# Optimization experiments

Measured on AMD Instinct MI355X. Metric: run time of the kernel, lower is better.

## Reference

```python
import jax, jax.numpy as jnp
import numpy as np

H = 4      # num_heads
D = 256    # hidden_dim
HD = 64    # head_dim
SCALE = HD ** -0.5


def setup_inputs() -> dict:
    key = jax.random.key(0)
    ks = jax.random.split(key, 5)
    x = jax.random.normal(ks[0], (4, 4096, D), dtype=jnp.float32)
    # Linear weights stored torch-style as [out, in]; y = x @ W.T
    init = 1.0 / np.sqrt(D)
    Wq = jax.random.uniform(ks[1], (D, D), jnp.float32, -init, init)
    Wk = jax.random.uniform(ks[2], (D, D), jnp.float32, -init, init)
    Wv = jax.random.uniform(ks[3], (D, D), jnp.float32, -init, init)
    Wo = jax.random.uniform(ks[4], (D, D), jnp.float32, -init, init)
    return {"x": x, "Wq": Wq, "Wk": Wk, "Wv": Wv, "Wo": Wo}


def reference(x, Wq, Wk, Wv, Wo):
    B, S, _ = x.shape
    # projections (torch Linear: x @ W.T)
    q = (x @ Wq.T).reshape(B, S, H, HD).transpose(0, 2, 1, 3)  # [B,H,S,HD]
    k = (x @ Wk.T).reshape(B, S, H, HD).transpose(0, 2, 1, 3)
    v = (x @ Wv.T).reshape(B, S, H, HD).transpose(0, 2, 1, 3)
    scores = jnp.einsum('bhqd,bhkd->bhqk', q, k) * SCALE  # [B,H,S,S]
    causal = jnp.triu(jnp.ones((S, S), dtype=bool), k=1)
    scores = jnp.where(causal[None, None], -jnp.inf, scores)
    attn = jax.nn.softmax(scores, axis=-1)
    out = jnp.einsum('bhqk,bhkd->bhqd', attn, v)  # [B,H,S,HD]
    out = out.transpose(0, 2, 1, 3).reshape(B, S, D)
    return out @ Wo.T
```

## Files before the change

kernel.cpp:

```cpp
#include <hip/hip_runtime.h>
#include <hip/hip_bf16.h>
#include <cstdint>

using short8  = __attribute__((ext_vector_type(8))) short;
using u16x8   = __attribute__((ext_vector_type(8))) unsigned short;
using u16x4   = __attribute__((ext_vector_type(4))) unsigned short;
using f32x4   = __attribute__((ext_vector_type(4))) float;
using f32x16  = __attribute__((ext_vector_type(16))) float;

constexpr int BN = 4, HN = 4, SN = 4096, DN = 256, HD = 64;
constexpr int MROWS = BN * SN;
constexpr float QSCL = 0.18033688011112042f;

__device__ __forceinline__ unsigned short f2bf(float x) {
  union { float f; unsigned int u; } c; c.f = x;
  unsigned int u = c.u;
  return (unsigned short)((u + 0x7fffu + ((u >> 16) & 1u)) >> 16);
}
__device__ __forceinline__ float bf2f(unsigned short h) {
  union { unsigned int u; float f; } c; c.u = ((unsigned int)h) << 16;
  return c.f;
}
__device__ __forceinline__ unsigned int cvt_pk_bf16(float a, float b) {
  unsigned int r;
  asm("v_cvt_pk_bf16_f32 %0, %1, %2" : "=v"(r) : "v"(a), "v"(b));
  return r;
}
__device__ __forceinline__ void pl32swap(unsigned int& a, unsigned int& b) {
  asm volatile("v_permlane32_swap_b32 %0, %1" : "+v"(a), "+v"(b));
}

#define GLDS16(g, l)                                                  \
  __builtin_amdgcn_global_load_lds(                                   \
      (const __attribute__((address_space(1))) void*)(g),             \
      (__attribute__((address_space(3))) void*)(l), 16, 0, 0)

__global__ __launch_bounds__(256) void convert_kernel(
    const float* __restrict__ x,  const float* __restrict__ Wq,
    const float* __restrict__ Wk, const float* __restrict__ Wv,
    const float* __restrict__ Wo,
    unsigned short* __restrict__ xb, unsigned short* __restrict__ Wcat,
    unsigned short* __restrict__ Wob) {
  const long NX4 = (long)MROWS * DN / 4;
  const long NW4 = 65536 / 4;
  const long total = NX4 + 4 * NW4;
  for (long i = (long)blockIdx.x * 256 + threadIdx.x; i < total;
       i += (long)gridDim.x * 256) {
    const float* src; unsigned short* dst;
    if (i < NX4) { src = x + i * 4; dst = xb + i * 4; }
    else {
      long j = i - NX4; int w = (int)(j >> 14); long o = (j & 16383) * 4;
      src = (w == 0 ? Wq : w == 1 ? Wk : w == 2 ? Wv : Wo) + o;
      dst = (w < 3 ? Wcat + (long)w * 65536 : Wob) + o;
    }
    float4 v = *(const float4*)src;
    u16x4 pk; pk[0] = f2bf(v.x); pk[1] = f2bf(v.y);
    pk[2] = f2bf(v.z); pk[3] = f2bf(v.w);
    *(u16x4*)dst = pk;
  }
}

template <int MODE, int NBN>
__global__ __launch_bounds__(256) void gemm_kernel(
    const unsigned short* __restrict__ Abf,
    const unsigned short* __restrict__ Bbf,
    unsigned short* __restrict__ qo, unsigned short* __restrict__ ko,
    unsigned short* __restrict__ vo, float* __restrict__ out) {
  constexpr int SMEM = (MODE == 1) ? 128 * 132 * 4 : 128 * 136 * 2;
  __shared__ __align__(16) char smem[SMEM];
  unsigned short* stg = (unsigned short*)smem;

  const int tid = threadIdx.x, lane = tid & 63, wid = tid >> 6;
  const int lo = lane & 15, hi = lane >> 4;
  const int bn = blockIdx.x % NBN, bm = blockIdx.x / NBN;
  const int wm = (wid >> 1) * 64, wn = (wid & 1) * 64;
  const long arow0 = (long)bm * 128, brow0 = (long)bn * 128;

  auto stage = [&](int buf, int kt) {
    const int row = (wid * 2) * 16 + (lane >> 2);
    const int col = (lane & 3) * 8;
    const unsigned short* ga = Abf + (arow0 + row) * DN + kt * 32 + col;
    const unsigned short* gb = Bbf + (brow0 + row) * DN + kt * 32 + col;
    unsigned short* la = stg + buf * 8192 + wid * 1024;
    unsigned short* lb = la + 4096;
    GLDS16(ga, la);
    GLDS16(ga + 16 * DN, la + 512);
    GLDS16(gb, lb);
    GLDS16(gb + 16 * DN, lb + 512);
  };

  f32x4 acc[4][4];
#pragma unroll
  for (int a = 0; a < 4; ++a)
#pragma unroll
    for (int b = 0; b < 4; ++b)
#pragma unroll
      for (int e = 0; e < 4; ++e) acc[a][b][e] = 0.f;

  stage(0, 0);
#pragma unroll
  for (int kt = 0; kt < 8; ++kt) {
    const int buf = kt & 1;
    __syncthreads();
    if (kt < 7) stage(buf ^ 1, kt + 1);
    const unsigned short* sa = stg + buf * 8192;
    const unsigned short* sb = sa + 4096;
    short8 af[4], bf[4];
#pragma unroll
    for (int f = 0; f < 4; ++f) {
      af[f] = *(const short8*)(sa + (wm + f * 16 + lo) * 32 + hi * 8);
      bf[f] = *(const short8*)(sb + (wn + f * 16 + lo) * 32 + hi * 8);
    }
#pragma unroll
    for (int fn = 0; fn < 4; ++fn)
#pragma unroll
      for (int fm = 0; fm < 4; ++fm)
        acc[fn][fm] = __builtin_amdgcn_mfma_f32_16x16x32_bf16(
            bf[fn], af[fm], acc[fn][fm], 0, 0, 0);
  }
  __syncthreads();

  if constexpr (MODE == 0) {
    unsigned short* cs = (unsigned short*)smem;
    if (bn < 4) {
      const float cscl = (bn < 2) ? QSCL : 1.0f;
#pragma unroll
      for (int fn = 0; fn < 4; ++fn)
#pragma unroll
        for (int fm = 0; fm < 4; ++fm) {
          u16x4 pk;
#pragma unroll
          for (int r = 0; r < 4; ++r) pk[r] = f2bf(acc[fn][fm][r] * cscl);
          const int m = wm + fm * 16 + lo, n0 = wn + fn * 16 + hi * 4;
          *(u16x4*)(cs + m * 136 + n0) = pk;
        }
      __syncthreads();
      unsigned short* dstmat = (bn < 2) ? qo : ko;
      const int colbase = (bn & 1) * 128;
#pragma unroll
      for (int p = 0; p < 8; ++p) {
        const int ml = p * 16 + (tid >> 4), n0 = (tid & 15) * 8;
        u16x8 v = *(u16x8*)(cs + ml * 136 + n0);
        const int c = colbase + n0, h = c >> 6, hd = c & 63;
        const long m = arow0 + ml;
        const int b = (int)(m >> 12), s = (int)(m & 4095);
        *(u16x8*)(dstmat + ((long)(b * HN + h) * SN + s) * HD + hd) = v;
      }
    } else {
#pragma unroll
      for (int fn = 0; fn < 4; ++fn)
#pragma unroll
        for (int fm = 0; fm < 4; ++fm) {
          const int m = wm + fm * 16 + lo, n0 = wn + fn * 16 + hi * 4;
#pragma unroll
          for (int r = 0; r < 4; ++r)
            cs[(n0 + r) * 136 + m] = f2bf(acc[fn][fm][r]);
        }
      __syncthreads();
      const int b = (int)(arow0 >> 12), sbase = (int)(arow0 & 4095);
#pragma unroll
      for (int p = 0; p < 8; ++p) {
        const int cl = p * 16 + (tid >> 4);
        const int s0 = (tid & 15) * 8;
        u16x8 v = *(u16x8*)(cs + cl * 136 + s0);
        const int c = (bn & 1) * 128 + cl, h = c >> 6, hd = c & 63;
        *(u16x8*)(vo + ((long)((b * HN + h) * HD + hd)) * SN + sbase + s0) = v;
      }
    }
  } else {
    float* csf = (float*)smem;
#pragma unroll
    for (int fn = 0; fn < 4; ++fn)
#pragma unroll
      for (int fm = 0; fm < 4; ++fm) {
        const int m = wm + fm * 16 + lo, n0 = wn + fn * 16 + hi * 4;
        *(f32x4*)(csf + m * 132 + n0) = acc[fn][fm];
      }
    __syncthreads();
#pragma unroll
    for (int p = 0; p < 8; ++p) {
      const int ml = p * 16 + (tid >> 4), n0 = (tid & 15) * 8;
      f32x4 v0 = *(f32x4*)(csf + ml * 132 + n0);
      f32x4 v1 = *(f32x4*)(csf + ml * 132 + n0 + 4);
      float* dst = out + (arow0 + ml) * DN + bn * 128 + n0;
      *(f32x4*)dst = v0;
      *(f32x4*)(dst + 4) = v1;
    }
  }
}

template <int NSPLIT>
__global__ __launch_bounds__(256, 2) void attn_kernel(
    const unsigned short* __restrict__ Qw, const unsigned short* __restrict__ Kw,
    const unsigned short* __restrict__ VTp, unsigned short* __restrict__ Ow,
    unsigned short* __restrict__ Op, float* __restrict__ Mp,
    float* __restrict__ Lp) {
  __shared__ __align__(16) unsigned short sK[2][4096];
  __shared__ __align__(16) unsigned short sV[2][4096];

  const int tid = threadIdx.x;
  const int w = tid >> 6, lane = tid & 63;
  const int l31 = lane & 31, h5 = lane >> 5;
  const int bid = blockIdx.x;
  const int bh = (bid & 7) * 2 + ((bid >> 3) & 1);
  int c, g;
  if constexpr (NSPLIT == 2) { c = (bid >> 4) & 1; g = bid >> 5; }
  else { c = 0; g = bid >> 4; }
  const int t = 31 - g;
  const int q0 = t * 128;
  const int qw = q0 + w * 32;
  const long base = (long)bh * SN * HD;
  const int tlast = 2 * t + 1;
  const int wlast = 2 * t + (w >> 1);

  const int sr = w * 16 + (lane >> 3);
  const int gcol8 = (((lane & 7) ^ (lane >> 3)) << 3);
  auto stage = [&](int buf, int k0) {
    const unsigned short* gk = Kw + base + (long)(k0 + sr) * HD + gcol8;
    GLDS16(gk, &sK[buf][w * 1024]);
    GLDS16(gk + 8 * HD, &sK[buf][w * 1024 + 512]);
    const unsigned short* gv = VTp + base + (long)sr * SN + k0 + gcol8;
    GLDS16(gv, &sV[buf][w * 1024]);
    GLDS16(gv + 8 * SN, &sV[buf][w * 1024 + 512]);
  };

  short8 qf[4];
#pragma unroll
  for (int ks = 0; ks < 4; ++ks)
    qf[ks] = *(const short8*)(Qw + base + (long)(qw + l31) * HD + ks * 16 + h5 * 8);

  f32x16 oacc[2];
#pragma unroll
  for (int oh = 0; oh < 2; ++oh)
#pragma unroll
    for (int r = 0; r < 16; ++r) oacc[oh][r] = 0.f;
  float m_ = -INFINITY, l_ = 0.f;

  const int swz = (l31 & 7) << 3;

  stage(0, c * 64);
  __syncthreads();
  int buf = 0;
  for (int kt = c; kt <= tlast; kt += NSPLIT) {
    if (kt + NSPLIT <= tlast) stage(buf ^ 1, (kt + NSPLIT) * 64);

    if (kt <= wlast) {
      const int k0 = kt * 64;
      short8 kb[8];
#pragma unroll
      for (int s = 0; s < 2; ++s)
#pragma unroll
        for (int ks = 0; ks < 4; ++ks)
          kb[s * 4 + ks] = *(const short8*)&sK[buf][(32 * s + l31) * 64 +
                                                   (((2 * ks + h5) << 3) ^ swz)];
      f32x16 c0, c1;
#pragma unroll
      for (int r = 0; r < 16; ++r) { c0[r] = 0.f; c1[r] = 0.f; }
#pragma unroll
      for (int ks = 0; ks < 4; ++ks)
        c0 = __builtin_amdgcn_mfma_f32_32x32x16_bf16(kb[ks], qf[ks], c0, 0, 0, 0);
#pragma unroll
      for (int ks = 0; ks < 4; ++ks)
        c1 = __builtin_amdgcn_mfma_f32_32x32x16_bf16(kb[4 + ks], qf[ks], c1, 0, 0, 0);

      short8 vt0[4], vt1[4];
#pragma unroll
      for (int ks = 0; ks < 4; ++ks) {
        const int col = ((2 * ks + h5) << 3) ^ swz;
        vt0[ks] = *(const short8*)&sV[buf][l31 * 64 + col];
        vt1[ks] = *(const short8*)&sV[buf][(32 + l31) * 64 + col];
      }

      if (kt == wlast) {
        const int mb0 = k0 + 4 * h5 - qw - l31;
#pragma unroll
        for (int r = 0; r < 16; ++r) {
          const int d = (r & 3) + 8 * (r >> 2);
          if (mb0 + d > 0)      c0[r] = -INFINITY;
          if (mb0 + 32 + d > 0) c1[r] = -INFINITY;
        }
      }

      float mv[16];
#pragma unroll
      for (int r = 0; r < 16; ++r) mv[r] = fmaxf(c0[r], c1[r]);
#pragma unroll
      for (int st = 8; st >= 1; st >>= 1)
#pragma unroll
        for (int i = 0; i < st; ++i) mv[i] = fmaxf(mv[i], mv[i + st]);
      const float mx = fmaxf(mv[0], __shfl_xor(mv[0], 32, 64));

      if (__any(mx > m_ + 11.5f)) {
        const float mn = fmaxf(m_, mx);
        const float alpha = __builtin_amdgcn_exp2f(m_ - mn);
        m_ = mn;
        l_ *= alpha;
#pragma unroll
        for (int oh = 0; oh < 2; ++oh)
#pragma unroll
          for (int r = 0; r < 16; ++r) oacc[oh][r] *= alpha;
      }

#pragma unroll
      for (int r = 0; r < 16; ++r) {
        c0[r] = __builtin_amdgcn_exp2f(c0[r] - m_);
        c1[r] = __builtin_amdgcn_exp2f(c1[r] - m_);
      }
      float sv[16];
#pragma unroll
      for (int r = 0; r < 16; ++r) sv[r] = c0[r] + c1[r];
#pragma unroll
      for (int st = 8; st >= 1; st >>= 1)
#pragma unroll
        for (int i = 0; i < st; ++i) sv[i] += sv[i + st];
      l_ += sv[0] + __shfl_xor(sv[0], 32, 64);

      short8 pb[4];
#pragma unroll
      for (int s = 0; s < 2; ++s)
#pragma unroll
        for (int u = 0; u < 2; ++u) {
          unsigned int a0, a1, b0, b1;
          if (s == 0) {
            a0 = cvt_pk_bf16(c0[8 * u + 0], c0[8 * u + 1]);
            a1 = cvt_pk_bf16(c0[8 * u + 2], c0[8 * u + 3]);
            b0 = cvt_pk_bf16(c0[8 * u + 4], c0[8 * u + 5]);
            b1 = cvt_pk_bf16(c0[8 * u + 6], c0[8 * u + 7]);
          } else {
            a0 = cvt_pk_bf16(c1[8 * u + 0], c1[8 * u + 1]);
            a1 = cvt_pk_bf16(c1[8 * u + 2], c1[8 * u + 3]);
            b0 = cvt_pk_bf16(c1[8 * u + 4], c1[8 * u + 5]);
            b1 = cvt_pk_bf16(c1[8 * u + 6], c1[8 * u + 7]);
          }
          pl32swap(a0, b0);
          pl32swap(a1, b1);
          union { unsigned int u4[4]; short8 v; } pu;
          pu.u4[0] = a0; pu.u4[1] = a1; pu.u4[2] = b0; pu.u4[3] = b1;
          pb[s * 2 + u] = pu.v;
        }

#pragma unroll
      for (int ks = 0; ks < 4; ++ks) {
        oacc[0] = __builtin_amdgcn_mfma_f32_32x32x16_bf16(vt0[ks], pb[ks], oacc[0], 0, 0, 0);
        oacc[1] = __builtin_amdgcn_mfma_f32_32x32x16_bf16(vt1[ks], pb[ks], oacc[1], 0, 0, 0);
      }
    }

    __syncthreads();
    buf ^= 1;
  }

  if constexpr (NSPLIT == 1) {
    unsigned short* ob = (unsigned short*)sK;
    const float rl = 1.f / l_;
#pragma unroll
    for (int oh = 0; oh < 2; ++oh)
#pragma unroll
      for (int rq = 0; rq < 4; ++rq) {
        const int hdb = 32 * oh + 8 * rq + 4 * h5;
        const unsigned int u0 = cvt_pk_bf16(oacc[oh][4 * rq + 0] * rl,
                                            oacc[oh][4 * rq + 1] * rl);
        const unsigned int u1 = cvt_pk_bf16(oacc[oh][4 * rq + 2] * rl,
                                            oacc[oh][4 * rq + 3] * rl);
        *(uint2*)&ob[w * 2048 + l31 * 64 + (hdb ^ ((l31 & 7) << 3))] =
            make_uint2(u0, u1);
      }
    __syncthreads();
    const int b = bh >> 2, h = bh & 3;
#pragma unroll
    for (int pass = 0; pass < 4; ++pass) {
      const int idx = pass * 256 + tid;
      const int row = idx >> 3, j = idx & 7;
      const int wreg = row >> 5, qi = row & 31;
      u16x8 vv = *(u16x8*)&ob[wreg * 2048 + qi * 64 +
                              ((j * 8) ^ ((qi & 7) << 3))];
      *(u16x8*)(Ow + ((long)(b * SN + q0 + row)) * DN + h * HD + j * 8) = vv;
    }
  } else {
    const long pb0 = (long)(c * 16 + bh) * 64;
#pragma unroll
    for (int oh = 0; oh < 2; ++oh)
#pragma unroll
      for (int rq = 0; rq < 4; ++rq)
#pragma unroll
        for (int e = 0; e < 4; ++e) {
          const int hd = 32 * oh + 8 * rq + 4 * h5 + e;
          Op[(pb0 + hd) * SN + qw + l31] = f2bf(oacc[oh][4 * rq + e]);
        }
    if (h5 == 0) {
      Mp[(long)(c * 16 + bh) * SN + qw + l31] = m_;
      Lp[(long)(c * 16 + bh) * SN + qw + l31] = l_;
    }
  }
}

template <int NS>
__global__ __launch_bounds__(256) void merge_kernel(
    const unsigned short* __restrict__ Op, const float* __restrict__ Mp,
    const float* __restrict__ Lp, unsigned short* __restrict__ Ow) {
  __shared__ float wsm[NS][64];
  __shared__ __align__(16) unsigned short obuf[64][72];
  const int tid = threadIdx.x;
  const int bh = blockIdx.x >> 6;
  const int qb = (blockIdx.x & 63) * 64;
  if (tid < 64) {
    const int q = qb + tid;
    float m[NS], l[NS];
    float ms = -INFINITY;
#pragma unroll
    for (int i = 0; i < NS; ++i) {
      m[i] = Mp[(long)(i * 16 + bh) * SN + q];
      l[i] = Lp[(long)(i * 16 + bh) * SN + q];
      ms = fmaxf(ms, m[i]);
    }
    float denom = 0.f, a[NS];
#pragma unroll
    for (int i = 0; i < NS; ++i) {
      a[i] = __builtin_amdgcn_exp2f(m[i] - ms);
      denom += l[i] * a[i];
    }
    const float rl = 1.f / denom;
#pragma unroll
    for (int i = 0; i < NS; ++i) wsm[i][tid] = a[i] * rl;
  }
  __syncthreads();
#pragma unroll
  for (int pass = 0; pass < 16; ++pass) {
    const int idx = pass * 256 + tid;
    const int hd = idx >> 6, q = idx & 63;
    float acc = 0.f;
#pragma unroll
    for (int i = 0; i < NS; ++i)
      acc += bf2f(Op[((long)(i * 16 + bh) * 64 + hd) * SN + qb + q]) * wsm[i][q];
    obuf[q][hd ^ ((q & 7) << 3)] = f2bf(acc);
  }
  __syncthreads();
  const int b = bh >> 2, h = bh & 3;
#pragma unroll
  for (int pass = 0; pass < 4; ++pass) {
    const int idx = pass * 256 + tid;
    const int q = idx >> 4, hg = (idx & 15) * 4;
    uint2 v = *(uint2*)&obuf[q][hg ^ ((q & 7) << 3)];
    *(uint2*)(Ow + ((long)(b * SN + qb + q)) * DN + h * HD + hg) = v;
  }
}

extern "C" void kernel_launch(void* const* d_in, const int* in_sizes, int n_in,
                              void* d_out, int out_size, void* d_ws, size_t ws_size,
                              hipStream_t stream) {
  const float* x  = (const float*)d_in[0];
  const float* Wq = (const float*)d_in[1];
  const float* Wk = (const float*)d_in[2];
  const float* Wv = (const float*)d_in[3];
  const float* Wo = (const float*)d_in[4];
  float* out = (float*)d_out;

  const size_t per = (size_t)MROWS * DN;
  unsigned short* xb   = (unsigned short*)d_ws;
  unsigned short* Wcat = xb + per;
  unsigned short* Wob  = Wcat + 768 * 256;
  unsigned short* Qw   = Wob + 65536;
  unsigned short* Kw   = Qw + per;
  unsigned short* VTw  = Kw + per;
  unsigned short* Ow   = xb;
  const size_t base_bytes = (4 * per + 768 * 256 + 65536) * sizeof(unsigned short);
  unsigned short* Op = (unsigned short*)((char*)d_ws + base_bytes);
  float* Mp = (float*)(Op + (size_t)2 * 16 * 64 * SN);
  float* Lp = Mp + (size_t)2 * 16 * SN;
  const size_t need = base_bytes +
      (size_t)2 * 16 * 64 * SN * sizeof(unsigned short) +
      2 * (size_t)2 * 16 * SN * sizeof(float);

  convert_kernel<<<2048, 256, 0, stream>>>(x, Wq, Wk, Wv, Wo, xb, Wcat, Wob);
  gemm_kernel<0, 6><<<6 * (MROWS / 128), 256, 0, stream>>>(
      xb, Wcat, Qw, Kw, VTw, nullptr);
  if (ws_size >= need) {
    attn_kernel<2><<<1024, 256, 0, stream>>>(Qw, Kw, VTw, nullptr, Op, Mp, Lp);
    merge_kernel<2><<<16 * (SN / 64), 256, 0, stream>>>(Op, Mp, Lp, Ow);
  } else {
    attn_kernel<1><<<512, 256, 0, stream>>>(
        Qw, Kw, VTw, Ow, nullptr, nullptr, nullptr);
  }
  gemm_kernel<1, 2><<<2 * (MROWS / 128), 256, 0, stream>>>(
      Ow, Wob, nullptr, nullptr, nullptr, out);
}
```

Before: 91.73 us.

## Give each attention wave two 32-row query tiles, halving block size

The attention kernel now runs 2 waves per block instead of 4, with each wave handling 64 query rows as two 32-row sub-tiles. The K and V fragments read from LDS are shared by both sub-tiles, which halves LDS fragment reads per unit of MFMA work. The staging loop is rewritten so 128 threads still load the full 64-row K/V tiles. The cost is roughly doubled accumulator and register pressure per wave, and fewer waves per CU to hide latency, which may reduce occupancy and increase causal-imbalance idling inside a block.

```diff
diff --git a/kernel.cpp b/kernel.cpp
--- a/kernel.cpp
+++ b/kernel.cpp
@@ -190,7 +190,7 @@
 }
 
 template <int NSPLIT>
-__global__ __launch_bounds__(256, 2) void attn_kernel(
+__global__ __launch_bounds__(128, 2) void attn_kernel(
     const unsigned short* __restrict__ Qw, const unsigned short* __restrict__ Kw,
     const unsigned short* __restrict__ VTp, unsigned short* __restrict__ Ow,
     unsigned short* __restrict__ Op, float* __restrict__ Mp,
@@ -208,35 +208,115 @@
   else { c = 0; g = bid >> 4; }
   const int t = 31 - g;
   const int q0 = t * 128;
-  const int qw = q0 + w * 32;
+  const int qA = q0 + w * 64, qB = qA + 32;
   const long base = (long)bh * SN * HD;
   const int tlast = 2 * t + 1;
-  const int wlast = 2 * t + (w >> 1);
-
-  const int sr = w * 16 + (lane >> 3);
-  const int gcol8 = (((lane & 7) ^ (lane >> 3)) << 3);
+  const int wlast = 2 * t + w;
+
+  const int r8 = lane >> 3;
+  const int gcol8 = (((lane & 7) ^ r8) << 3);
   auto stage = [&](int buf, int k0) {
-    const unsigned short* gk = Kw + base + (long)(k0 + sr) * HD + gcol8;
-    GLDS16(gk, &sK[buf][w * 1024]);
-    GLDS16(gk + 8 * HD, &sK[buf][w * 1024 + 512]);
-    const unsigned short* gv = VTp + base + (long)sr * SN + k0 + gcol8;
-    GLDS16(gv, &sV[buf][w * 1024]);
-    GLDS16(gv + 8 * SN, &sV[buf][w * 1024 + 512]);
+#pragma unroll
+    for (int i = 0; i < 4; ++i) {
+      const int row = w * 32 + i * 8;
+      GLDS16(Kw + base + (long)(k0 + row + r8) * HD + gcol8,
+             &sK[buf][row * 64]);
+      GLDS16(VTp + base + (long)(row + r8) * SN + k0 + gcol8,
+             &sV[buf][row * 64]);
+    }
   };
 
-  short8 qf[4];
-#pragma unroll
-  for (int ks = 0; ks < 4; ++ks)
-    qf[ks] = *(const short8*)(Qw + base + (long)(qw + l31) * HD + ks * 16 + h5 * 8);
-
-  f32x16 oacc[2];
-#pragma unroll
-  for (int oh = 0; oh < 2; ++oh)
-#pragma unroll
-    for (int r = 0; r < 16; ++r) oacc[oh][r] = 0.f;
-  float m_ = -INFINITY, l_ = 0.f;
+  short8 qfA[4], qfB[4];
+#pragma unroll
+  for (int ks = 0; ks < 4; ++ks) {
+    qfA[ks] = *(const short8*)(Qw + base + (long)(qA + l31) * HD + ks * 16 + h5 * 8);
+    qfB[ks] = *(const short8*)(Qw + base + (long)(qB + l31) * HD + ks * 16 + h5 * 8);
+  }
+
+  f32x16 oaccA[2], oaccB[2], zro;
+#pragma unroll
+  for (int r = 0; r < 16; ++r) zro[r] = 0.f;
+  oaccA[0] = zro; oaccA[1] = zro; oaccB[0] = zro; oaccB[1] = zro;
+  float mA = -INFINITY, lA = 0.f, mB = -INFINITY, lB = 0.f;
 
   const int swz = (l31 & 7) << 3;
+
+  auto softmax_pv = [&](f32x16& c0, f32x16& c1, float& m_, float& l_,
+                        f32x16* oacc, const short8* vt0, const short8* vt1,
+                        int kt, int k0, int qw) {
+    if (kt == wlast) {
+      const int mb0 = k0 + 4 * h5 - qw - l31;
+#pragma unroll
+      for (int r = 0; r < 16; ++r) {
+        const int d = (r & 3) + 8 * (r >> 2);
+        if (mb0 + d > 0)      c0[r] = -INFINITY;
+        if (mb0 + 32 + d > 0) c1[r] = -INFINITY;
+      }
+    }
+    float mv[16];
+#pragma unroll
+    for (int r = 0; r < 16; ++r) mv[r] = fmaxf(c0[r], c1[r]);
+#pragma unroll
+    for (int st = 8; st >= 1; st >>= 1)
+#pragma unroll
+      for (int i = 0; i < st; ++i) mv[i] = fmaxf(mv[i], mv[i + st]);
+    const float mx = fmaxf(mv[0], __shfl_xor(mv[0], 32, 64));
+
+    if (__any(mx > m_ + 11.5f)) {
+      const float mn = fmaxf(m_, mx);
+      const float alpha = __builtin_amdgcn_exp2f(m_ - mn);
+      m_ = mn;
+      l_ *= alpha;
+#pragma unroll
+      for (int oh = 0; oh < 2; ++oh)
+#pragma unroll
+        for (int r = 0; r < 16; ++r) oacc[oh][r] *= alpha;
+    }
+
+#pragma unroll
+    for (int r = 0; r < 16; ++r) {
+      c0[r] = __builtin_amdgcn_exp2f(c0[r] - m_);
+      c1[r] = __builtin_amdgcn_exp2f(c1[r] - m_);
+    }
+    float sv[16];
+#pragma unroll
+    for (int r = 0; r < 16; ++r) sv[r] = c0[r] + c1[r];
+#pragma unroll
+    for (int st = 8; st >= 1; st >>= 1)
+#pragma unroll
+      for (int i = 0; i < st; ++i) sv[i] += sv[i + st];
+    l_ += sv[0] + __shfl_xor(sv[0], 32, 64);
+
+    short8 pb[4];
+#pragma unroll
+    for (int s = 0; s < 2; ++s)
+#pragma unroll
+      for (int u = 0; u < 2; ++u) {
+        unsigned int a0, a1, b0, b1;
+        if (s == 0) {
+          a0 = cvt_pk_bf16(c0[8 * u + 0], c0[8 * u + 1]);
+          a1 = cvt_pk_bf16(c0[8 * u + 2], c0[8 * u + 3]);
+          b0 = cvt_pk_bf16(c0[8 * u + 4], c0[8 * u + 5]);
+          b1 = cvt_pk_bf16(c0[8 * u + 6], c0[8 * u + 7]);
+        } else {
+          a0 = cvt_pk_bf16(c1[8 * u + 0], c1[8 * u + 1]);
+          a1 = cvt_pk_bf16(c1[8 * u + 2], c1[8 * u + 3]);
+          b0 = cvt_pk_bf16(c1[8 * u + 4], c1[8 * u + 5]);
+          b1 = cvt_pk_bf16(c1[8 * u + 6], c1[8 * u + 7]);
+        }
+        pl32swap(a0, b0);
+        pl32swap(a1, b1);
+        union { unsigned int u4[4]; short8 v; } pu;
+        pu.u4[0] = a0; pu.u4[1] = a1; pu.u4[2] = b0; pu.u4[3] = b1;
+        pb[s * 2 + u] = pu.v;
+      }
+
+#pragma unroll
+    for (int ks = 0; ks < 4; ++ks) {
+      oacc[0] = __builtin_amdgcn_mfma_f32_32x32x16_bf16(vt0[ks], pb[ks], oacc[0], 0, 0, 0);
+      oacc[1] = __builtin_amdgcn_mfma_f32_32x32x16_bf16(vt1[ks], pb[ks], oacc[1], 0, 0, 0);
+    }
+  };
 
   stage(0, c * 64);
   __syncthreads();
@@ -253,15 +333,18 @@
         for (int ks = 0; ks < 4; ++ks)
           kb[s * 4 + ks] = *(const short8*)&sK[buf][(32 * s + l31) * 64 +
                                                    (((2 * ks + h5) << 3) ^ swz)];
-      f32x16 c0, c1;
-#pragma unroll
-      for (int r = 0; r < 16; ++r) { c0[r] = 0.f; c1[r] = 0.f; }
-#pragma unroll
-      for (int ks = 0; ks < 4; ++ks)
-        c0 = __builtin_amdgcn_mfma_f32_32x32x16_bf16(kb[ks], qf[ks], c0, 0, 0, 0);
-#pragma unroll
-      for (int ks = 0; ks < 4; ++ks)
-        c1 = __builtin_amdgcn_mfma_f32_32x32x16_bf16(kb[4 + ks], qf[ks], c1, 0, 0, 0);
+      f32x16 cA0, cA1, cB0, cB1;
+      cA0 = __builtin_amdgcn_mfma_f32_32x32x16_bf16(kb[0], qfA[0], zro, 0, 0, 0);
+      cA1 = __builtin_amdgcn_mfma_f32_32x32x16_bf16(kb[4], qfA[0], zro, 0, 0, 0);
+      cB0 = __builtin_amdgcn_mfma_f32_32x32x16_bf16(kb[0], qfB[0], zro, 0, 0, 0);
+      cB1 = __builtin_amdgcn_mfma_f32_32x32x16_bf16(kb[4], qfB[0], zro, 0, 0, 0);
+#pragma unroll
+      for (int ks = 1; ks < 4; ++ks) {
+        cA0 = __builtin_amdgcn_mfma_f32_32x32x16_bf16(kb[ks], qfA[ks], cA0, 0, 0, 0);
+        cA1 = __builtin_amdgcn_mfma_f32_32x32x16_bf16(kb[4 + ks], qfA[ks], cA1, 0, 0, 0);
+        cB0 = __builtin_amdgcn_mfma_f32_32x32x16_bf16(kb[ks], qfB[ks], cB0, 0, 0, 0);
+        cB1 = __builtin_amdgcn_mfma_f32_32x32x16_bf16(kb[4 + ks], qfB[ks], cB1, 0, 0, 0);
+      }
 
       short8 vt0[4], vt1[4];
 #pragma unroll
@@ -271,79 +354,8 @@
         vt1[ks] = *(const short8*)&sV[buf][(32 + l31) * 64 + col];
       }
 
-      if (kt == wlast) {
-        const int mb0 = k0 + 4 * h5 - qw - l31;
-#pragma unroll
-        for (int r = 0; r < 16; ++r) {
-          const int d = (r & 3) + 8 * (r >> 2);
-          if (mb0 + d > 0)      c0[r] = -INFINITY;
-          if (mb0 + 32 + d > 0) c1[r] = -INFINITY;
-        }
-      }
-
-      float mv[16];
-#pragma unroll
-      for (int r = 0; r < 16; ++r) mv[r] = fmaxf(c0[r], c1[r]);
-#pragma unroll
-      for (int st = 8; st >= 1; st >>= 1)
-#pragma unroll
-        for (int i = 0; i < st; ++i) mv[i] = fmaxf(mv[i], mv[i + st]);
-      const float mx = fmaxf(mv[0], __shfl_xor(mv[0], 32, 64));
-
-      if (__any(mx > m_ + 11.5f)) {
-        const float mn = fmaxf(m_, mx);
-        const float alpha = __builtin_amdgcn_exp2f(m_ - mn);
-        m_ = mn;
-        l_ *= alpha;
-#pragma unroll
-        for (int oh = 0; oh < 2; ++oh)
-#pragma unroll
-          for (int r = 0; r < 16; ++r) oacc[oh][r] *= alpha;
-      }
-
-#pragma unroll
-      for (int r = 0; r < 16; ++r) {
-        c0[r] = __builtin_amdgcn_exp2f(c0[r] - m_);
-        c1[r] = __builtin_amdgcn_exp2f(c1[r] - m_);
-      }
-      float sv[16];
-#pragma unroll
-      for (int r = 0; r < 16; ++r) sv[r] = c0[r] + c1[r];
-#pragma unroll
-      for (int st = 8; st >= 1; st >>= 1)
-#pragma unroll
-        for (int i = 0; i < st; ++i) sv[i] += sv[i + st];
-      l_ += sv[0] + __shfl_xor(sv[0], 32, 64);
-
-      short8 pb[4];
-#pragma unroll
-      for (int s = 0; s < 2; ++s)
-#pragma unroll
-        for (int u = 0; u < 2; ++u) {
-          unsigned int a0, a1, b0, b1;
-          if (s == 0) {
-            a0 = cvt_pk_bf16(c0[8 * u + 0], c0[8 * u + 1]);
-            a1 = cvt_pk_bf16(c0[8 * u + 2], c0[8 * u + 3]);
-            b0 = cvt_pk_bf16(c0[8 * u + 4], c0[8 * u + 5]);
-            b1 = cvt_pk_bf16(c0[8 * u + 6], c0[8 * u + 7]);
-          } else {
-            a0 = cvt_pk_bf16(c1[8 * u + 0], c1[8 * u + 1]);
-            a1 = cvt_pk_bf16(c1[8 * u + 2], c1[8 * u + 3]);
-            b0 = cvt_pk_bf16(c1[8 * u + 4], c1[8 * u + 5]);
-            b1 = cvt_pk_bf16(c1[8 * u + 6], c1[8 * u + 7]);
-          }
-          pl32swap(a0, b0);
-          pl32swap(a1, b1);
-          union { unsigned int u4[4]; short8 v; } pu;
-          pu.u4[0] = a0; pu.u4[1] = a1; pu.u4[2] = b0; pu.u4[3] = b1;
-          pb[s * 2 + u] = pu.v;
-        }
-
-#pragma unroll
-      for (int ks = 0; ks < 4; ++ks) {
-        oacc[0] = __builtin_amdgcn_mfma_f32_32x32x16_bf16(vt0[ks], pb[ks], oacc[0], 0, 0, 0);
-        oacc[1] = __builtin_amdgcn_mfma_f32_32x32x16_bf16(vt1[ks], pb[ks], oacc[1], 0, 0, 0);
-      }
+      softmax_pv(cA0, cA1, mA, lA, oaccA, vt0, vt1, kt, k0, qA);
+      softmax_pv(cB0, cB1, mB, lB, oaccB, vt0, vt1, kt, k0, qB);
     }
 
     __syncthreads();
@@ -352,44 +364,54 @@
 
   if constexpr (NSPLIT == 1) {
     unsigned short* ob = (unsigned short*)sK;
-    const float rl = 1.f / l_;
-#pragma unroll
-    for (int oh = 0; oh < 2; ++oh)
-#pragma unroll
-      for (int rq = 0; rq < 4; ++rq) {
-        const int hdb = 32 * oh + 8 * rq + 4 * h5;
-        const unsigned int u0 = cvt_pk_bf16(oacc[oh][4 * rq + 0] * rl,
-                                            oacc[oh][4 * rq + 1] * rl);
-        const unsigned int u1 = cvt_pk_bf16(oacc[oh][4 * rq + 2] * rl,
-                                            oacc[oh][4 * rq + 3] * rl);
-        *(uint2*)&ob[w * 2048 + l31 * 64 + (hdb ^ ((l31 & 7) << 3))] =
-            make_uint2(u0, u1);
-      }
+    const float rlA = 1.f / lA, rlB = 1.f / lB;
+#pragma unroll
+    for (int s = 0; s < 2; ++s) {
+      const f32x16* oacc = s ? oaccB : oaccA;
+      const float rl = s ? rlB : rlA;
+      const int rowb = w * 64 + s * 32 + l31;
+#pragma unroll
+      for (int oh = 0; oh < 2; ++oh)
+#pragma unroll
+        for (int rq = 0; rq < 4; ++rq) {
+          const int hdb = 32 * oh + 8 * rq + 4 * h5;
+          const unsigned int u0 = cvt_pk_bf16(oacc[oh][4 * rq + 0] * rl,
+                                              oacc[oh][4 * rq + 1] * rl);
+          const unsigned int u1 = cvt_pk_bf16(oacc[oh][4 * rq + 2] * rl,
+                                              oacc[oh][4 * rq + 3] * rl);
+          *(uint2*)&ob[rowb * 64 + (hdb ^ ((l31 & 7) << 3))] = make_uint2(u0, u1);
+        }
+    }
     __syncthreads();
     const int b = bh >> 2, h = bh & 3;
 #pragma unroll
-    for (int pass = 0; pass < 4; ++pass) {
-      const int idx = pass * 256 + tid;
+    for (int pass = 0; pass < 8; ++pass) {
+      const int idx = pass * 128 + tid;
       const int row = idx >> 3, j = idx & 7;
-      const int wreg = row >> 5, qi = row & 31;
-      u16x8 vv = *(u16x8*)&ob[wreg * 2048 + qi * 64 +
-                              ((j * 8) ^ ((qi & 7) << 3))];
+      u16x8 vv = *(u16x8*)&ob[row * 64 + ((j * 8) ^ ((row & 7) << 3))];
       *(u16x8*)(Ow + ((long)(b * SN + q0 + row)) * DN + h * HD + j * 8) = vv;
     }
   } else {
     const long pb0 = (long)(c * 16 + bh) * 64;
 #pragma unroll
-    for (int oh = 0; oh < 2; ++oh)
-#pragma unroll
-      for (int rq = 0; rq < 4; ++rq)
-#pragma unroll
-        for (int e = 0; e < 4; ++e) {
-          const int hd = 32 * oh + 8 * rq + 4 * h5 + e;
-          Op[(pb0 + hd) * SN + qw + l31] = f2bf(oacc[oh][4 * rq + e]);
-        }
+    for (int s = 0; s < 2; ++s) {
+      const f32x16* oacc = s ? oaccB : oaccA;
+      const int qw = s ? qB : qA;
+#pragma unroll
+      for (int oh = 0; oh < 2; ++oh)
+#pragma unroll
+        for (int rq = 0; rq < 4; ++rq)
+#pragma unroll
+          for (int e = 0; e < 4; ++e) {
+            const int hd = 32 * oh + 8 * rq + 4 * h5 + e;
+            Op[(pb0 + hd) * SN + qw + l31] = f2bf(oacc[oh][4 * rq + e]);
+          }
+    }
     if (h5 == 0) {
-      Mp[(long)(c * 16 + bh) * SN + qw + l31] = m_;
-      Lp[(long)(c * 16 + bh) * SN + qw + l31] = l_;
+      Mp[(long)(c * 16 + bh) * SN + qA + l31] = mA;
+      Lp[(long)(c * 16 + bh) * SN + qA + l31] = lA;
+      Mp[(long)(c * 16 + bh) * SN + qB + l31] = mB;
+      Lp[(long)(c * 16 + bh) * SN + qB + l31] = lB;
     }
   }
 }
@@ -475,10 +497,10 @@
   gemm_kernel<0, 6><<<6 * (MROWS / 128), 256, 0, stream>>>(
       xb, Wcat, Qw, Kw, VTw, nullptr);
   if (ws_size >= need) {
-    attn_kernel<2><<<1024, 256, 0, stream>>>(Qw, Kw, VTw, nullptr, Op, Mp, Lp);
+    attn_kernel<2><<<1024, 128, 0, stream>>>(Qw, Kw, VTw, nullptr, Op, Mp, Lp);
     merge_kernel<2><<<16 * (SN / 64), 256, 0, stream>>>(Op, Mp, Lp, Ow);
   } else {
-    attn_kernel<1><<<512, 256, 0, stream>>>(
+    attn_kernel<1><<<512, 128, 0, stream>>>(
         Qw, Kw, VTw, Ow, nullptr, nullptr, nullptr);
   }
   gemm_kernel<1, 2><<<2 * (MROWS / 128), 256, 0, stream>>>(
```

New measurement: 116.8 us. 1.27x slower.
